# Performance work log

Hardware: AMD Instinct MI355X
Metric: run time of the kernel (lower is better)

The kernel has to match this reference:

```python
import jax, jax.numpy as jnp
import numpy as np

NUM_GRAPHS = 1024
N_NODES = 8388608

def setup_inputs() -> dict:
    key = jax.random.key(0)
    k1, k2, k3 = jax.random.split(key, 3)
    positions = jax.random.normal(k1, (N_NODES, 3), dtype=jnp.float32)
    q = jax.random.normal(k2, (N_NODES,), dtype=jnp.float32)
    batch = jnp.sort(jax.random.randint(k3, (N_NODES,), 0, NUM_GRAPHS, dtype=jnp.int64))
    return {"positions": positions, "q": q, "batch": batch}

def reference(positions, q, batch):
    # q: [N] -> [N,1]; remove global mean over all nodes (remove_mean=True)
    qc = q[:, None] - jnp.mean(q)
    # per-graph polarization: sum_i q_i * r_i  -> [NUM_GRAPHS, 3]
    pol = jax.ops.segment_sum(qc * positions, batch, num_segments=NUM_GRAPHS)
    return pol
```

## Files before the change

### kernel.cpp

```cpp
#include <hip/hip_runtime.h>


#define N_NODES         8388608
#define NUM_GRAPHS      1024
#define BLK             256
#define NODES_PER_BLOCK 4096
#define NBLOCKS         (N_NODES / NODES_PER_BLOCK)
#define ITER            4
#define NSLOT           4

#define IBASE_OFF       16
#define SPLIT_OFF       2064
#define REC_OFF         10256
#define REC_STRIDE      32
#define EXTRA_OFF       (REC_OFF + NBLOCKS * REC_STRIDE)
#define WS_FLOATS       (EXTRA_OFF + NUM_GRAPHS * 6)

__global__ __launch_bounds__(BLK) void split_kernel(const int* __restrict__ batch,
                                                    float* __restrict__ ws) {
    int b = blockIdx.x * BLK + threadIdx.x;
    if (b >= NBLOCKS) return;

    float* extra = ws + EXTRA_OFF;
    extra[b * 3 + 0] = 0.f; extra[b * 3 + 1] = 0.f; extra[b * 3 + 2] = 0.f;

    const int s = b * NODES_PER_BLOCK;
    const int e = s + NODES_PER_BLOCK;
    int i0 = batch[s];
    int i1 = batch[e - 1];
    int split = e;
    if (i1 != i0) {
        int lo = s + 1, hi = e - 1;
        while (lo < hi) {
            int mid = (lo + hi) >> 1;
            if (batch[mid] > i0) hi = mid; else lo = mid + 1;
        }
        split = lo;
    }
    ((int4*)(ws + SPLIT_OFF))[b] = make_int4(i0, i1, split, 0);
    ((int*)(ws + IBASE_OFF))[b] = i0;
}

__global__ __launch_bounds__(BLK) void pol_main(const float4* __restrict__ p4,
                                                const float4* __restrict__ q4,
                                                const int*    __restrict__ batch,
                                                float* __restrict__ ws) {
    __shared__ float sslot[NSLOT * 6];
    __shared__ float sqsum;

    const int t = threadIdx.x;
    const int b = blockIdx.x;
    float* extra = ws + EXTRA_OFF;

    const int e = (b + 1) * NODES_PER_BLOCK;
    const int4 si = ((const int4*)(ws + SPLIT_OFF))[b];
    const int i0 = si.x, i1 = si.y, split = si.z;
    const bool general = (i1 > i0 + 1);

    if (t < NSLOT * 6) sslot[t] = 0.f;
    if (t == 0) sqsum = 0.f;
    __syncthreads();

    float4 Q[ITER], P0[ITER], P1[ITER], P2[ITER];
    const int blk_v4 = b * (NODES_PER_BLOCK / 4);
    #pragma unroll
    for (int j = 0; j < ITER; ++j) {
        int vi = blk_v4 + j * BLK + t;
        Q[j]  = q4[vi];
        P0[j] = p4[3 * vi + 0];
        P1[j] = p4[3 * vi + 1];
        P2[j] = p4[3 * vi + 2];
    }

    float aqx = 0, aqy = 0, aqz = 0, arx = 0, ary = 0, arz = 0;
    float bqx = 0, bqy = 0, bqz = 0, brx = 0, bry = 0, brz = 0;
    float qsum = 0.f;

    if (!general) {
        #pragma unroll
        for (int j = 0; j < ITER; ++j) {
            int gidx = (blk_v4 + j * BLK + t) * 4;
            float qs[4] = {Q[j].x, Q[j].y, Q[j].z, Q[j].w};
            float px[4] = {P0[j].x, P0[j].w, P1[j].z, P2[j].y};
            float py[4] = {P0[j].y, P1[j].x, P1[j].w, P2[j].z};
            float pz[4] = {P0[j].z, P1[j].y, P2[j].x, P2[j].w};
            qsum += (qs[0] + qs[1]) + (qs[2] + qs[3]);
            #pragma unroll
            for (int k = 0; k < 4; ++k) {
                if (gidx + k < split) {
                    aqx = fmaf(qs[k], px[k], aqx); aqy = fmaf(qs[k], py[k], aqy);
                    aqz = fmaf(qs[k], pz[k], aqz);
                    arx += px[k]; ary += py[k]; arz += pz[k];
                } else {
                    bqx = fmaf(qs[k], px[k], bqx); bqy = fmaf(qs[k], py[k], bqy);
                    bqz = fmaf(qs[k], pz[k], bqz);
                    brx += px[k]; bry += py[k]; brz += pz[k];
                }
            }
        }
    } else {
        #pragma unroll
        for (int j = 0; j < ITER; ++j) {
            int gidx = (blk_v4 + j * BLK + t) * 4;
            float qs[4] = {Q[j].x, Q[j].y, Q[j].z, Q[j].w};
            float px[4] = {P0[j].x, P0[j].w, P1[j].z, P2[j].y};
            float py[4] = {P0[j].y, P1[j].x, P1[j].w, P2[j].z};
            float pz[4] = {P0[j].z, P1[j].y, P2[j].x, P2[j].w};
            for (int k = 0; k < 4; ++k) {
                int id = batch[gidx + k];
                float qv = qs[k];
                qsum += qv;
                atomicAdd(&extra[id * 6 + 0], qv * px[k]);
                atomicAdd(&extra[id * 6 + 1], qv * py[k]);
                atomicAdd(&extra[id * 6 + 2], qv * pz[k]);
                atomicAdd(&extra[id * 6 + 3], px[k]);
                atomicAdd(&extra[id * 6 + 4], py[k]);
                atomicAdd(&extra[id * 6 + 5], pz[k]);
            }
        }
    }

    #pragma unroll
    for (int off = 32; off > 0; off >>= 1) qsum += __shfl_down(qsum, off, 64);
    if ((t & 63) == 0) atomicAdd(&sqsum, qsum);

    if (!general) {
        #pragma unroll
        for (int off = 32; off > 0; off >>= 1) {
            aqx += __shfl_down(aqx, off, 64); aqy += __shfl_down(aqy, off, 64);
            aqz += __shfl_down(aqz, off, 64); arx += __shfl_down(arx, off, 64);
            ary += __shfl_down(ary, off, 64); arz += __shfl_down(arz, off, 64);
        }
        if ((t & 63) == 0) {
            atomicAdd(&sslot[0], aqx); atomicAdd(&sslot[1], aqy);
            atomicAdd(&sslot[2], aqz); atomicAdd(&sslot[3], arx);
            atomicAdd(&sslot[4], ary); atomicAdd(&sslot[5], arz);
        }
        if (split < e) {
            #pragma unroll
            for (int off = 32; off > 0; off >>= 1) {
                bqx += __shfl_down(bqx, off, 64); bqy += __shfl_down(bqy, off, 64);
                bqz += __shfl_down(bqz, off, 64); brx += __shfl_down(brx, off, 64);
                bry += __shfl_down(bry, off, 64); brz += __shfl_down(brz, off, 64);
            }
            if ((t & 63) == 0) {
                int sl = i1 - i0;
                atomicAdd(&sslot[sl * 6 + 0], bqx); atomicAdd(&sslot[sl * 6 + 1], bqy);
                atomicAdd(&sslot[sl * 6 + 2], bqz); atomicAdd(&sslot[sl * 6 + 3], brx);
                atomicAdd(&sslot[sl * 6 + 4], bry); atomicAdd(&sslot[sl * 6 + 5], brz);
            }
        }
    }
    __syncthreads();

    float* rec = ws + REC_OFF + (size_t)b * REC_STRIDE;
    if (t == 0) rec[0] = sqsum;
    if (t < NSLOT * 6) rec[8 + t] = sslot[t];
}

__global__ __launch_bounds__(1024) void finalize_kernel(const float* __restrict__ ws,
                                                        float* __restrict__ out) {
    __shared__ float sm[16];
    __shared__ float smean;
    const int t = threadIdx.x;

    float s = ws[REC_OFF + (size_t)t * REC_STRIDE]
            + ws[REC_OFF + (size_t)(t + 1024) * REC_STRIDE];
    #pragma unroll
    for (int off = 32; off > 0; off >>= 1) s += __shfl_down(s, off, 64);
    if ((t & 63) == 0) sm[t >> 6] = s;
    __syncthreads();
    if (t == 0) {
        float tot = 0.f;
        #pragma unroll
        for (int i = 0; i < 16; ++i) tot += sm[i];
        smean = tot * (1.0f / (float)N_NODES);
    }
    __syncthreads();
    const float mean = smean;

    const int g = t;
    const int* ibase = (const int*)(ws + IBASE_OFF);
    const float* extra = ws + EXTRA_OFF;

    float qx = extra[g * 6 + 0], qy = extra[g * 6 + 1], qz = extra[g * 6 + 2];
    float rx = extra[g * 6 + 3], ry = extra[g * 6 + 4], rz = extra[g * 6 + 5];

    int lo = 0, hi = NBLOCKS - 1, B = -1;
    while (lo <= hi) {
        int mid = (lo + hi) >> 1;
        if (ibase[mid] <= g) { B = mid; lo = mid + 1; } else hi = mid - 1;
    }
    for (int b = B; b >= 0; --b) {
        int sl = g - ibase[b];
        if (sl >= NSLOT) break;
        const float* p = ws + REC_OFF + (size_t)b * REC_STRIDE + 8 + sl * 6;
        qx += p[0]; qy += p[1]; qz += p[2];
        rx += p[3]; ry += p[4]; rz += p[5];
    }
    out[g * 3 + 0] = fmaf(-mean, rx, qx);
    out[g * 3 + 1] = fmaf(-mean, ry, qy);
    out[g * 3 + 2] = fmaf(-mean, rz, qz);
}


__global__ void sum_q_kernel(const float* __restrict__ q, float* __restrict__ ws, int n4) {
    int tid = blockIdx.x * blockDim.x + threadIdx.x;
    int stride = gridDim.x * blockDim.x;
    const float4* q4 = (const float4*)q;
    float s = 0.f;
    for (int i = tid; i < n4; i += stride) {
        float4 v = q4[i];
        s += (v.x + v.y) + (v.z + v.w);
    }
    for (int off = 32; off > 0; off >>= 1) s += __shfl_down(s, off, 64);
    __shared__ float smem[4];
    int lane = threadIdx.x & 63, wave = threadIdx.x >> 6;
    if (lane == 0) smem[wave] = s;
    __syncthreads();
    if (threadIdx.x == 0) atomicAdd(ws, (smem[0] + smem[1]) + (smem[2] + smem[3]));
}

__global__ void pol_atomic_kernel(const float* __restrict__ pos,
                                  const float* __restrict__ q,
                                  const int*   __restrict__ batch,
                                  const float* __restrict__ ws,
                                  float* __restrict__ out, int n) {
    const float mean = ws[0] * (1.0f / (float)N_NODES);
    int tid = blockIdx.x * blockDim.x + threadIdx.x;
    int stride = gridDim.x * blockDim.x;
    int n4 = n >> 2;
    const float4* q4 = (const float4*)q;
    const int4*   b4 = (const int4*)batch;
    const float4* p4 = (const float4*)pos;

    for (int i = tid; i < n4; i += stride) {
        float4 qv = q4[i];
        int4   bv = b4[i];
        float4 p0 = p4[3 * i + 0];
        float4 p1 = p4[3 * i + 1];
        float4 p2 = p4[3 * i + 2];
        float qs[4] = {qv.x - mean, qv.y - mean, qv.z - mean, qv.w - mean};
        int  ids[4] = {bv.x, bv.y, bv.z, bv.w};
        float px[4] = {p0.x, p0.w, p1.z, p2.y};
        float py[4] = {p0.y, p1.x, p1.w, p2.z};
        float pz[4] = {p0.z, p1.y, p2.x, p2.w};
        int cur = ids[0];
        float sx = 0.f, sy = 0.f, sz = 0.f;
        #pragma unroll
        for (int j = 0; j < 4; ++j) {
            if (ids[j] != cur) {
                atomicAdd(&out[cur * 3 + 0], sx);
                atomicAdd(&out[cur * 3 + 1], sy);
                atomicAdd(&out[cur * 3 + 2], sz);
                sx = sy = sz = 0.f;
                cur = ids[j];
            }
            sx = fmaf(qs[j], px[j], sx);
            sy = fmaf(qs[j], py[j], sy);
            sz = fmaf(qs[j], pz[j], sz);
        }
        int first = __shfl(cur, 0, 64);
        bool uniform = __all(cur == first);
        if (uniform) {
            for (int off = 32; off > 0; off >>= 1) {
                sx += __shfl_down(sx, off, 64);
                sy += __shfl_down(sy, off, 64);
                sz += __shfl_down(sz, off, 64);
            }
            if ((threadIdx.x & 63) == 0) {
                atomicAdd(&out[cur * 3 + 0], sx);
                atomicAdd(&out[cur * 3 + 1], sy);
                atomicAdd(&out[cur * 3 + 2], sz);
            }
        } else {
            atomicAdd(&out[cur * 3 + 0], sx);
            atomicAdd(&out[cur * 3 + 1], sy);
            atomicAdd(&out[cur * 3 + 2], sz);
        }
    }
}

extern "C" void kernel_launch(void* const* d_in, const int* in_sizes, int n_in,
                              void* d_out, int out_size, void* d_ws, size_t ws_size,
                              hipStream_t stream) {
    const float* pos   = (const float*)d_in[0];
    const float* q     = (const float*)d_in[1];
    const int*   batch = (const int*)d_in[2];
    float* out = (float*)d_out;
    float* ws  = (float*)d_ws;
    int n = in_sizes[1];

    if (ws_size >= (size_t)WS_FLOATS * sizeof(float)) {
        split_kernel<<<NBLOCKS / BLK, BLK, 0, stream>>>(batch, ws);
        pol_main<<<NBLOCKS, BLK, 0, stream>>>((const float4*)pos, (const float4*)q,
                                              batch, ws);
        finalize_kernel<<<1, 1024, 0, stream>>>(ws, out);
    } else {
        hipMemsetAsync(d_out, 0, (size_t)out_size * sizeof(float), stream);
        hipMemsetAsync(d_ws, 0, sizeof(float), stream);
        sum_q_kernel<<<4096, BLK, 0, stream>>>(q, ws, n >> 2);
        pol_atomic_kernel<<<8192, BLK, 0, stream>>>(pos, q, batch, ws, out, n);
    }
}
```

Baseline: 204.5 us.

## Restructure per-wave loads to contiguous float4 streams with phase-based accumulation

In the common case (at most two graphs per block), each wave now owns a contiguous 1024-node region. It reads positions as consecutive float4s, so each lane does one coalesced load per iteration instead of three strided ones. The matching q values are fetched by index m/3, and xyz components are accumulated into three phase-indexed float4 accumulators that are recombined at the end. Loads are double-buffered across three groups, and a separate mixed path handles a region containing the graph boundary. The aim is better coalescing and lower register pressure, at the cost of extra select arithmetic and redundant q loads.

```diff
diff --git a/kernel.cpp b/kernel.cpp
--- a/kernel.cpp
+++ b/kernel.cpp
@@ -16,11 +16,21 @@
 #define EXTRA_OFF       (REC_OFF + NBLOCKS * REC_STRIDE)
 #define WS_FLOATS       (EXTRA_OFF + NUM_GRAPHS * 6)
 
+__device__ __forceinline__ float4 f4z() { return make_float4(0.f, 0.f, 0.f, 0.f); }
+__device__ __forceinline__ float4 f4add(float4 a, float4 b) {
+    return make_float4(a.x + b.x, a.y + b.y, a.z + b.z, a.w + b.w);
+}
+__device__ __forceinline__ float4 f4mul(float4 a, float4 b) {
+    return make_float4(a.x * b.x, a.y * b.y, a.z * b.z, a.w * b.w);
+}
+__device__ __forceinline__ float4 f4sel(bool c, float4 a) {
+    return make_float4(c ? a.x : 0.f, c ? a.y : 0.f, c ? a.z : 0.f, c ? a.w : 0.f);
+}
+
 __global__ __launch_bounds__(BLK) void split_kernel(const int* __restrict__ batch,
                                                     float* __restrict__ ws) {
     int b = blockIdx.x * BLK + threadIdx.x;
     if (b >= NBLOCKS) return;
-
     float* extra = ws + EXTRA_OFF;
     extra[b * 3 + 0] = 0.f; extra[b * 3 + 1] = 0.f; extra[b * 3 + 2] = 0.f;
 
@@ -41,6 +51,27 @@
     ((int*)(ws + IBASE_OFF))[b] = i0;
 }
 
+__device__ __forceinline__ void flush_seg(int id, int base,
+                                          float qx, float qy, float qz,
+                                          float rx, float ry, float rz,
+                                          float* sslot, float* extra) {
+    int s = id - base;
+    if (s >= 0 && s < NSLOT) {
+        atomicAdd(&sslot[s * 6 + 0], qx); atomicAdd(&sslot[s * 6 + 1], qy);
+        atomicAdd(&sslot[s * 6 + 2], qz); atomicAdd(&sslot[s * 6 + 3], rx);
+        atomicAdd(&sslot[s * 6 + 4], ry); atomicAdd(&sslot[s * 6 + 5], rz);
+    } else {
+        atomicAdd(&extra[id * 6 + 0], qx); atomicAdd(&extra[id * 6 + 1], qy);
+        atomicAdd(&extra[id * 6 + 2], qz); atomicAdd(&extra[id * 6 + 3], rx);
+        atomicAdd(&extra[id * 6 + 4], ry); atomicAdd(&extra[id * 6 + 5], rz);
+    }
+}
+
+#define PHACC(a0, a1, a2, u) \
+    { a0 = f4add(a0, f4sel(ph == 0, u)); \
+      a1 = f4add(a1, f4sel(ph == 1, u)); \
+      a2 = f4add(a2, f4sel(ph == 2, u)); }
+
 __global__ __launch_bounds__(BLK) void pol_main(const float4* __restrict__ p4,
                                                 const float4* __restrict__ q4,
                                                 const int*    __restrict__ batch,
@@ -52,7 +83,6 @@
     const int b = blockIdx.x;
     float* extra = ws + EXTRA_OFF;
 
-    const int e = (b + 1) * NODES_PER_BLOCK;
     const int4 si = ((const int4*)(ws + SPLIT_OFF))[b];
     const int i0 = si.x, i1 = si.y, split = si.z;
     const bool general = (i1 > i0 + 1);
@@ -61,58 +91,144 @@
     if (t == 0) sqsum = 0.f;
     __syncthreads();
 
-    float4 Q[ITER], P0[ITER], P1[ITER], P2[ITER];
-    const int blk_v4 = b * (NODES_PER_BLOCK / 4);
-    #pragma unroll
-    for (int j = 0; j < ITER; ++j) {
-        int vi = blk_v4 + j * BLK + t;
-        Q[j]  = q4[vi];
-        P0[j] = p4[3 * vi + 0];
-        P1[j] = p4[3 * vi + 1];
-        P2[j] = p4[3 * vi + 2];
-    }
-
-    float aqx = 0, aqy = 0, aqz = 0, arx = 0, ary = 0, arz = 0;
-    float bqx = 0, bqy = 0, bqz = 0, brx = 0, bry = 0, brz = 0;
     float qsum = 0.f;
 
     if (!general) {
+        const int lane   = t & 63;
+        const int region = b * 4 + (t >> 6);
+        const int n0     = region * 1024;
+        const int Wp     = region * 768;
+        const bool allB  = (split <= n0);
+        const bool mixed = (split > n0) && (split < n0 + 1024);
+        const int fsplit = split * 3;
+
+        float4 V0[4], Q0[4], V1[4], Q1[4];
+        auto ldg = [&](float4* Vv, float4* Qv, int g) {
+            #pragma unroll
+            for (int k2 = 0; k2 < 4; ++k2) {
+                int m = Wp + lane + 64 * (g * 4 + k2);
+                Vv[k2] = p4[m];
+                Qv[k2] = q4[(unsigned)m / 3u];
+            }
+        };
+
+        float4 qrA0 = f4z(), qrA1 = f4z(), qrA2 = f4z();
+        float4 rA0  = f4z(), rA1  = f4z(), rA2  = f4z();
+        float4 qrB0 = f4z(), qrB1 = f4z(), qrB2 = f4z();
+        float4 rB0  = f4z(), rB1  = f4z(), rB2  = f4z();
+
+        auto comp_pure = [&](const float4* Vv, const float4* Qv, int g) {
+            #pragma unroll
+            for (int k2 = 0; k2 < 4; ++k2) {
+                int m = Wp + lane + 64 * (g * 4 + k2);
+                int s3 = (int)((unsigned)m / 3u);
+                int ph = m - 3 * s3;
+                float4 v = Vv[k2], qq = Qv[k2];
+                float4 qv;
+                qv.x = ph == 0 ? qq.x : (ph == 1 ? qq.y : qq.z);
+                qv.y = ph == 0 ? qq.x : (ph == 1 ? qq.y : qq.w);
+                qv.z = ph == 0 ? qq.x : (ph == 1 ? qq.z : qq.w);
+                qv.w = ph == 0 ? qq.y : (ph == 1 ? qq.z : qq.w);
+                qsum += (ph == 0) ? (qq.x + qq.y) + (qq.z + qq.w) : 0.f;
+                float4 u = f4mul(v, qv);
+                PHACC(qrA0, qrA1, qrA2, u);
+                PHACC(rA0, rA1, rA2, v);
+            }
+        };
+        auto comp_mixed = [&](const float4* Vv, const float4* Qv, int g) {
+            #pragma unroll
+            for (int k2 = 0; k2 < 4; ++k2) {
+                int m = Wp + lane + 64 * (g * 4 + k2);
+                int s3 = (int)((unsigned)m / 3u);
+                int ph = m - 3 * s3;
+                float4 v = Vv[k2], qq = Qv[k2];
+                float4 qv;
+                qv.x = ph == 0 ? qq.x : (ph == 1 ? qq.y : qq.z);
+                qv.y = ph == 0 ? qq.x : (ph == 1 ? qq.y : qq.w);
+                qv.z = ph == 0 ? qq.x : (ph == 1 ? qq.z : qq.w);
+                qv.w = ph == 0 ? qq.y : (ph == 1 ? qq.z : qq.w);
+                qsum += (ph == 0) ? (qq.x + qq.y) + (qq.z + qq.w) : 0.f;
+                int f0 = 4 * m;
+                float4 vA;
+                vA.x = (f0 + 0 < fsplit) ? v.x : 0.f;
+                vA.y = (f0 + 1 < fsplit) ? v.y : 0.f;
+                vA.z = (f0 + 2 < fsplit) ? v.z : 0.f;
+                vA.w = (f0 + 3 < fsplit) ? v.w : 0.f;
+                float4 vB = make_float4(v.x - vA.x, v.y - vA.y, v.z - vA.z, v.w - vA.w);
+                float4 uA = f4mul(vA, qv);
+                float4 uB = f4mul(vB, qv);
+                PHACC(qrA0, qrA1, qrA2, uA);
+                PHACC(rA0, rA1, rA2, vA);
+                PHACC(qrB0, qrB1, qrB2, uB);
+                PHACC(rB0, rB1, rB2, vB);
+            }
+        };
+
+        ldg(V0, Q0, 0);
+        ldg(V1, Q1, 1);
+        if (!mixed) {
+            comp_pure(V0, Q0, 0);
+            ldg(V0, Q0, 2);
+            comp_pure(V1, Q1, 1);
+            comp_pure(V0, Q0, 2);
+        } else {
+            comp_mixed(V0, Q0, 0);
+            ldg(V0, Q0, 2);
+            comp_mixed(V1, Q1, 1);
+            comp_mixed(V0, Q0, 2);
+        }
+
+        float AX = qrA0.x + qrA0.w + qrA1.z + qrA2.y;
+        float AY = qrA0.y + qrA1.x + qrA1.w + qrA2.z;
+        float AZ = qrA0.z + qrA1.y + qrA2.x + qrA2.w;
+        float ARX = rA0.x + rA0.w + rA1.z + rA2.y;
+        float ARY = rA0.y + rA1.x + rA1.w + rA2.z;
+        float ARZ = rA0.z + rA1.y + rA2.x + rA2.w;
         #pragma unroll
+        for (int off = 32; off > 0; off >>= 1) {
+            AX += __shfl_down(AX, off, 64);  AY += __shfl_down(AY, off, 64);
+            AZ += __shfl_down(AZ, off, 64);  ARX += __shfl_down(ARX, off, 64);
+            ARY += __shfl_down(ARY, off, 64); ARZ += __shfl_down(ARZ, off, 64);
+        }
+        if (lane == 0) {
+            int gid = (!mixed && allB) ? i1 : i0;
+            flush_seg(gid, i0, AX, AY, AZ, ARX, ARY, ARZ, sslot, extra);
+        }
+        if (mixed) {
+            float BX = qrB0.x + qrB0.w + qrB1.z + qrB2.y;
+            float BY = qrB0.y + qrB1.x + qrB1.w + qrB2.z;
+            float BZ = qrB0.z + qrB1.y + qrB2.x + qrB2.w;
+            float BRX = rB0.x + rB0.w + rB1.z + rB2.y;
+            float BRY = rB0.y + rB1.x + rB1.w + rB2.z;
+            float BRZ = rB0.z + rB1.y + rB2.x + rB2.w;
+            #pragma unroll
+            for (int off = 32; off > 0; off >>= 1) {
+                BX += __shfl_down(BX, off, 64);  BY += __shfl_down(BY, off, 64);
+                BZ += __shfl_down(BZ, off, 64);  BRX += __shfl_down(BRX, off, 64);
+                BRY += __shfl_down(BRY, off, 64); BRZ += __shfl_down(BRZ, off, 64);
+            }
+            if (lane == 0)
+                flush_seg(i1, i0, BX, BY, BZ, BRX, BRY, BRZ, sslot, extra);
+        }
+    } else {
+        const int blk_v4 = b * (NODES_PER_BLOCK / 4);
         for (int j = 0; j < ITER; ++j) {
-            int gidx = (blk_v4 + j * BLK + t) * 4;
-            float qs[4] = {Q[j].x, Q[j].y, Q[j].z, Q[j].w};
-            float px[4] = {P0[j].x, P0[j].w, P1[j].z, P2[j].y};
-            float py[4] = {P0[j].y, P1[j].x, P1[j].w, P2[j].z};
-            float pz[4] = {P0[j].z, P1[j].y, P2[j].x, P2[j].w};
-            qsum += (qs[0] + qs[1]) + (qs[2] + qs[3]);
-            #pragma unroll
+            int vi = blk_v4 + j * BLK + t;
+            float4 qv = q4[vi];
+            float4 p0 = p4[3 * vi + 0];
+            float4 p1 = p4[3 * vi + 1];
+            float4 p2 = p4[3 * vi + 2];
+            float qs[4] = {qv.x, qv.y, qv.z, qv.w};
+            float px[4] = {p0.x, p0.w, p1.z, p2.y};
+            float py[4] = {p0.y, p1.x, p1.w, p2.z};
+            float pz[4] = {p0.z, p1.y, p2.x, p2.w};
             for (int k = 0; k < 4; ++k) {
-                if (gidx + k < split) {
-                    aqx = fmaf(qs[k], px[k], aqx); aqy = fmaf(qs[k], py[k], aqy);
-                    aqz = fmaf(qs[k], pz[k], aqz);
-                    arx += px[k]; ary += py[k]; arz += pz[k];
-                } else {
-                    bqx = fmaf(qs[k], px[k], bqx); bqy = fmaf(qs[k], py[k], bqy);
-                    bqz = fmaf(qs[k], pz[k], bqz);
-                    brx += px[k]; bry += py[k]; brz += pz[k];
-                }
-            }
-        }
-    } else {
-        #pragma unroll
-        for (int j = 0; j < ITER; ++j) {
-            int gidx = (blk_v4 + j * BLK + t) * 4;
-            float qs[4] = {Q[j].x, Q[j].y, Q[j].z, Q[j].w};
-            float px[4] = {P0[j].x, P0[j].w, P1[j].z, P2[j].y};
-            float py[4] = {P0[j].y, P1[j].x, P1[j].w, P2[j].z};
-            float pz[4] = {P0[j].z, P1[j].y, P2[j].x, P2[j].w};
-            for (int k = 0; k < 4; ++k) {
-                int id = batch[gidx + k];
-                float qv = qs[k];
-                qsum += qv;
-                atomicAdd(&extra[id * 6 + 0], qv * px[k]);
-                atomicAdd(&extra[id * 6 + 1], qv * py[k]);
-                atomicAdd(&extra[id * 6 + 2], qv * pz[k]);
+                int id = batch[vi * 4 + k];
+                float qj = qs[k];
+                qsum += qj;
+                atomicAdd(&extra[id * 6 + 0], qj * px[k]);
+                atomicAdd(&extra[id * 6 + 1], qj * py[k]);
+                atomicAdd(&extra[id * 6 + 2], qj * pz[k]);
                 atomicAdd(&extra[id * 6 + 3], px[k]);
                 atomicAdd(&extra[id * 6 + 4], py[k]);
                 atomicAdd(&extra[id * 6 + 5], pz[k]);
@@ -123,34 +239,6 @@
     #pragma unroll
     for (int off = 32; off > 0; off >>= 1) qsum += __shfl_down(qsum, off, 64);
     if ((t & 63) == 0) atomicAdd(&sqsum, qsum);
-
-    if (!general) {
-        #pragma unroll
-        for (int off = 32; off > 0; off >>= 1) {
-            aqx += __shfl_down(aqx, off, 64); aqy += __shfl_down(aqy, off, 64);
-            aqz += __shfl_down(aqz, off, 64); arx += __shfl_down(arx, off, 64);
-            ary += __shfl_down(ary, off, 64); arz += __shfl_down(arz, off, 64);
-        }
-        if ((t & 63) == 0) {
-            atomicAdd(&sslot[0], aqx); atomicAdd(&sslot[1], aqy);
-            atomicAdd(&sslot[2], aqz); atomicAdd(&sslot[3], arx);
-            atomicAdd(&sslot[4], ary); atomicAdd(&sslot[5], arz);
-        }
-        if (split < e) {
-            #pragma unroll
-            for (int off = 32; off > 0; off >>= 1) {
-                bqx += __shfl_down(bqx, off, 64); bqy += __shfl_down(bqy, off, 64);
-                bqz += __shfl_down(bqz, off, 64); brx += __shfl_down(brx, off, 64);
-                bry += __shfl_down(bry, off, 64); brz += __shfl_down(brz, off, 64);
-            }
-            if ((t & 63) == 0) {
-                int sl = i1 - i0;
-                atomicAdd(&sslot[sl * 6 + 0], bqx); atomicAdd(&sslot[sl * 6 + 1], bqy);
-                atomicAdd(&sslot[sl * 6 + 2], bqz); atomicAdd(&sslot[sl * 6 + 3], brx);
-                atomicAdd(&sslot[sl * 6 + 4], bry); atomicAdd(&sslot[sl * 6 + 5], brz);
-            }
-        }
-    }
     __syncthreads();
 
     float* rec = ws + REC_OFF + (size_t)b * REC_STRIDE;
```

Measured after the change: 206.9 us. No clear change (+1.2%).

## Shrink tiles to 1024 nodes and add per-wave pure-segment fast path

Applied to the files above, without the earlier changes.

Each block now handles 1024 nodes with one float4 load per thread instead of 4096 nodes in four unrolled iterations, which quadruples the grid to 8192 blocks. The goal is more parallelism and less register pressure and latency per block. Waves whose 256 nodes sit entirely on one side of the segment split skip the per-element branch and reduce a single accumulator set. The workspace layout and the finalize loop are resized to match. The cost is four times as many per-tile records and a longer ibase binary search in finalize.

```diff
diff --git a/kernel.cpp b/kernel.cpp
--- a/kernel.cpp
+++ b/kernel.cpp
@@ -1,31 +1,30 @@
 #include <hip/hip_runtime.h>
 
 
-#define N_NODES         8388608
-#define NUM_GRAPHS      1024
-#define BLK             256
-#define NODES_PER_BLOCK 4096
-#define NBLOCKS         (N_NODES / NODES_PER_BLOCK)
-#define ITER            4
-#define NSLOT           4
-
-#define IBASE_OFF       16
-#define SPLIT_OFF       2064
-#define REC_OFF         10256
-#define REC_STRIDE      32
-#define EXTRA_OFF       (REC_OFF + NBLOCKS * REC_STRIDE)
-#define WS_FLOATS       (EXTRA_OFF + NUM_GRAPHS * 6)
+#define N_NODES     8388608
+#define NUM_GRAPHS  1024
+#define BLK         256
+#define TILE_NODES  1024
+#define NT          (N_NODES / TILE_NODES)
+#define NSLOT       4
+
+#define IBASE_OFF   16
+#define SPLIT_OFF   (IBASE_OFF + NT)
+#define REC_OFF     (SPLIT_OFF + 4 * NT)
+#define REC_STRIDE  32
+#define EXTRA_OFF   (REC_OFF + NT * REC_STRIDE)
+#define WS_FLOATS   (EXTRA_OFF + NUM_GRAPHS * 6)
 
 __global__ __launch_bounds__(BLK) void split_kernel(const int* __restrict__ batch,
                                                     float* __restrict__ ws) {
     int b = blockIdx.x * BLK + threadIdx.x;
-    if (b >= NBLOCKS) return;
-
-    float* extra = ws + EXTRA_OFF;
-    extra[b * 3 + 0] = 0.f; extra[b * 3 + 1] = 0.f; extra[b * 3 + 2] = 0.f;
-
-    const int s = b * NODES_PER_BLOCK;
-    const int e = s + NODES_PER_BLOCK;
+    if (b >= NT) return;
+    if (b < 2048) {
+        float* extra = ws + EXTRA_OFF;
+        extra[b * 3 + 0] = 0.f; extra[b * 3 + 1] = 0.f; extra[b * 3 + 2] = 0.f;
+    }
+    const int s = b * TILE_NODES;
+    const int e = s + TILE_NODES;
     int i0 = batch[s];
     int i1 = batch[e - 1];
     int split = e;
@@ -41,6 +40,22 @@
     ((int*)(ws + IBASE_OFF))[b] = i0;
 }
 
+__device__ __forceinline__ void flush_seg(int id, int base,
+                                          float qx, float qy, float qz,
+                                          float rx, float ry, float rz,
+                                          float* sslot, float* extra) {
+    int s = id - base;
+    if (s >= 0 && s < NSLOT) {
+        atomicAdd(&sslot[s * 6 + 0], qx); atomicAdd(&sslot[s * 6 + 1], qy);
+        atomicAdd(&sslot[s * 6 + 2], qz); atomicAdd(&sslot[s * 6 + 3], rx);
+        atomicAdd(&sslot[s * 6 + 4], ry); atomicAdd(&sslot[s * 6 + 5], rz);
+    } else {
+        atomicAdd(&extra[id * 6 + 0], qx); atomicAdd(&extra[id * 6 + 1], qy);
+        atomicAdd(&extra[id * 6 + 2], qz); atomicAdd(&extra[id * 6 + 3], rx);
+        atomicAdd(&extra[id * 6 + 4], ry); atomicAdd(&extra[id * 6 + 5], rz);
+    }
+}
+
 __global__ __launch_bounds__(BLK) void pol_main(const float4* __restrict__ p4,
                                                 const float4* __restrict__ q4,
                                                 const int*    __restrict__ batch,
@@ -52,42 +67,56 @@
     const int b = blockIdx.x;
     float* extra = ws + EXTRA_OFF;
 
-    const int e = (b + 1) * NODES_PER_BLOCK;
+    if (t < NSLOT * 6) sslot[t] = 0.f;
+    if (t == 0) sqsum = 0.f;
+    __syncthreads();
+
     const int4 si = ((const int4*)(ws + SPLIT_OFF))[b];
+    const int vi = b * (TILE_NODES / 4) + t;
+    float4 qv = q4[vi];
+    float4 p0 = p4[3 * vi + 0];
+    float4 p1 = p4[3 * vi + 1];
+    float4 p2 = p4[3 * vi + 2];
+
     const int i0 = si.x, i1 = si.y, split = si.z;
     const bool general = (i1 > i0 + 1);
 
-    if (t < NSLOT * 6) sslot[t] = 0.f;
-    if (t == 0) sqsum = 0.f;
-    __syncthreads();
-
-    float4 Q[ITER], P0[ITER], P1[ITER], P2[ITER];
-    const int blk_v4 = b * (NODES_PER_BLOCK / 4);
-    #pragma unroll
-    for (int j = 0; j < ITER; ++j) {
-        int vi = blk_v4 + j * BLK + t;
-        Q[j]  = q4[vi];
-        P0[j] = p4[3 * vi + 0];
-        P1[j] = p4[3 * vi + 1];
-        P2[j] = p4[3 * vi + 2];
-    }
-
-    float aqx = 0, aqy = 0, aqz = 0, arx = 0, ary = 0, arz = 0;
-    float bqx = 0, bqy = 0, bqz = 0, brx = 0, bry = 0, brz = 0;
-    float qsum = 0.f;
+    const int lane   = t & 63;
+    const int wstart = b * TILE_NODES + (t >> 6) * 256;
+
+    float qs[4] = {qv.x, qv.y, qv.z, qv.w};
+    float px[4] = {p0.x, p0.w, p1.z, p2.y};
+    float py[4] = {p0.y, p1.x, p1.w, p2.z};
+    float pz[4] = {p0.z, p1.y, p2.x, p2.w};
+    float qsum = (qs[0] + qs[1]) + (qs[2] + qs[3]);
 
     if (!general) {
-        #pragma unroll
-        for (int j = 0; j < ITER; ++j) {
-            int gidx = (blk_v4 + j * BLK + t) * 4;
-            float qs[4] = {Q[j].x, Q[j].y, Q[j].z, Q[j].w};
-            float px[4] = {P0[j].x, P0[j].w, P1[j].z, P2[j].y};
-            float py[4] = {P0[j].y, P1[j].x, P1[j].w, P2[j].z};
-            float pz[4] = {P0[j].z, P1[j].y, P2[j].x, P2[j].w};
-            qsum += (qs[0] + qs[1]) + (qs[2] + qs[3]);
+        const bool pure = (split <= wstart) || (split >= wstart + 256);
+        if (pure) {
+            float ax = 0, ay = 0, az = 0, rx = 0, ry = 0, rz = 0;
             #pragma unroll
             for (int k = 0; k < 4; ++k) {
-                if (gidx + k < split) {
+                ax = fmaf(qs[k], px[k], ax); ay = fmaf(qs[k], py[k], ay);
+                az = fmaf(qs[k], pz[k], az);
+                rx += px[k]; ry += py[k]; rz += pz[k];
+            }
+            #pragma unroll
+            for (int off = 32; off > 0; off >>= 1) {
+                ax += __shfl_down(ax, off, 64); ay += __shfl_down(ay, off, 64);
+                az += __shfl_down(az, off, 64); rx += __shfl_down(rx, off, 64);
+                ry += __shfl_down(ry, off, 64); rz += __shfl_down(rz, off, 64);
+            }
+            if (lane == 0) {
+                int id = (split <= wstart) ? i1 : i0;
+                flush_seg(id, i0, ax, ay, az, rx, ry, rz, sslot, extra);
+            }
+        } else {
+            float aqx = 0, aqy = 0, aqz = 0, arx = 0, ary = 0, arz = 0;
+            float bqx = 0, bqy = 0, bqz = 0, brx = 0, bry = 0, brz = 0;
+            const int n0 = vi * 4;
+            #pragma unroll
+            for (int k = 0; k < 4; ++k) {
+                if (n0 + k < split) {
                     aqx = fmaf(qs[k], px[k], aqx); aqy = fmaf(qs[k], py[k], aqy);
                     aqz = fmaf(qs[k], pz[k], aqz);
                     arx += px[k]; ary += py[k]; arz += pz[k];
@@ -97,60 +126,36 @@
                     brx += px[k]; bry += py[k]; brz += pz[k];
                 }
             }
-        }
-    } else {
-        #pragma unroll
-        for (int j = 0; j < ITER; ++j) {
-            int gidx = (blk_v4 + j * BLK + t) * 4;
-            float qs[4] = {Q[j].x, Q[j].y, Q[j].z, Q[j].w};
-            float px[4] = {P0[j].x, P0[j].w, P1[j].z, P2[j].y};
-            float py[4] = {P0[j].y, P1[j].x, P1[j].w, P2[j].z};
-            float pz[4] = {P0[j].z, P1[j].y, P2[j].x, P2[j].w};
-            for (int k = 0; k < 4; ++k) {
-                int id = batch[gidx + k];
-                float qv = qs[k];
-                qsum += qv;
-                atomicAdd(&extra[id * 6 + 0], qv * px[k]);
-                atomicAdd(&extra[id * 6 + 1], qv * py[k]);
-                atomicAdd(&extra[id * 6 + 2], qv * pz[k]);
-                atomicAdd(&extra[id * 6 + 3], px[k]);
-                atomicAdd(&extra[id * 6 + 4], py[k]);
-                atomicAdd(&extra[id * 6 + 5], pz[k]);
-            }
-        }
-    }
-
-    #pragma unroll
-    for (int off = 32; off > 0; off >>= 1) qsum += __shfl_down(qsum, off, 64);
-    if ((t & 63) == 0) atomicAdd(&sqsum, qsum);
-
-    if (!general) {
-        #pragma unroll
-        for (int off = 32; off > 0; off >>= 1) {
-            aqx += __shfl_down(aqx, off, 64); aqy += __shfl_down(aqy, off, 64);
-            aqz += __shfl_down(aqz, off, 64); arx += __shfl_down(arx, off, 64);
-            ary += __shfl_down(ary, off, 64); arz += __shfl_down(arz, off, 64);
-        }
-        if ((t & 63) == 0) {
-            atomicAdd(&sslot[0], aqx); atomicAdd(&sslot[1], aqy);
-            atomicAdd(&sslot[2], aqz); atomicAdd(&sslot[3], arx);
-            atomicAdd(&sslot[4], ary); atomicAdd(&sslot[5], arz);
-        }
-        if (split < e) {
             #pragma unroll
             for (int off = 32; off > 0; off >>= 1) {
+                aqx += __shfl_down(aqx, off, 64); aqy += __shfl_down(aqy, off, 64);
+                aqz += __shfl_down(aqz, off, 64); arx += __shfl_down(arx, off, 64);
+                ary += __shfl_down(ary, off, 64); arz += __shfl_down(arz, off, 64);
                 bqx += __shfl_down(bqx, off, 64); bqy += __shfl_down(bqy, off, 64);
                 bqz += __shfl_down(bqz, off, 64); brx += __shfl_down(brx, off, 64);
                 bry += __shfl_down(bry, off, 64); brz += __shfl_down(brz, off, 64);
             }
-            if ((t & 63) == 0) {
-                int sl = i1 - i0;
-                atomicAdd(&sslot[sl * 6 + 0], bqx); atomicAdd(&sslot[sl * 6 + 1], bqy);
-                atomicAdd(&sslot[sl * 6 + 2], bqz); atomicAdd(&sslot[sl * 6 + 3], brx);
-                atomicAdd(&sslot[sl * 6 + 4], bry); atomicAdd(&sslot[sl * 6 + 5], brz);
-            }
-        }
-    }
+            if (lane == 0) {
+                flush_seg(i0, i0, aqx, aqy, aqz, arx, ary, arz, sslot, extra);
+                flush_seg(i1, i0, bqx, bqy, bqz, brx, bry, brz, sslot, extra);
+            }
+        }
+    } else {
+        const int n0 = vi * 4;
+        for (int k = 0; k < 4; ++k) {
+            int id = batch[n0 + k];
+            atomicAdd(&extra[id * 6 + 0], qs[k] * px[k]);
+            atomicAdd(&extra[id * 6 + 1], qs[k] * py[k]);
+            atomicAdd(&extra[id * 6 + 2], qs[k] * pz[k]);
+            atomicAdd(&extra[id * 6 + 3], px[k]);
+            atomicAdd(&extra[id * 6 + 4], py[k]);
+            atomicAdd(&extra[id * 6 + 5], pz[k]);
+        }
+    }
+
+    #pragma unroll
+    for (int off = 32; off > 0; off >>= 1) qsum += __shfl_down(qsum, off, 64);
+    if (lane == 0) atomicAdd(&sqsum, qsum);
     __syncthreads();
 
     float* rec = ws + REC_OFF + (size_t)b * REC_STRIDE;
@@ -164,8 +169,8 @@
     __shared__ float smean;
     const int t = threadIdx.x;
 
-    float s = ws[REC_OFF + (size_t)t * REC_STRIDE]
-            + ws[REC_OFF + (size_t)(t + 1024) * REC_STRIDE];
+    float s = 0.f;
+    for (int i = t; i < NT; i += 1024) s += ws[REC_OFF + (size_t)i * REC_STRIDE];
     #pragma unroll
     for (int off = 32; off > 0; off >>= 1) s += __shfl_down(s, off, 64);
     if ((t & 63) == 0) sm[t >> 6] = s;
@@ -186,7 +191,7 @@
     float qx = extra[g * 6 + 0], qy = extra[g * 6 + 1], qz = extra[g * 6 + 2];
     float rx = extra[g * 6 + 3], ry = extra[g * 6 + 4], rz = extra[g * 6 + 5];
 
-    int lo = 0, hi = NBLOCKS - 1, B = -1;
+    int lo = 0, hi = NT - 1, B = -1;
     while (lo <= hi) {
         int mid = (lo + hi) >> 1;
         if (ibase[mid] <= g) { B = mid; lo = mid + 1; } else hi = mid - 1;
@@ -292,9 +297,9 @@
     int n = in_sizes[1];
 
     if (ws_size >= (size_t)WS_FLOATS * sizeof(float)) {
-        split_kernel<<<NBLOCKS / BLK, BLK, 0, stream>>>(batch, ws);
-        pol_main<<<NBLOCKS, BLK, 0, stream>>>((const float4*)pos, (const float4*)q,
-                                              batch, ws);
+        split_kernel<<<NT / BLK, BLK, 0, stream>>>(batch, ws);
+        pol_main<<<NT, BLK, 0, stream>>>((const float4*)pos, (const float4*)q,
+                                         batch, ws);
         finalize_kernel<<<1, 1024, 0, stream>>>(ws, out);
     } else {
         hipMemsetAsync(d_out, 0, (size_t)out_size * sizeof(float), stream);
```

After: 244.2 us. 1.19x slower.
